# Optimization experiments

Hardware: AMD Instinct MI355X
Metric: run time of the kernel (lower is better)

## Reference

```python
import jax, jax.numpy as jnp
import numpy as np

EPS = 1e-5

def setup_inputs() -> dict:
    key = jax.random.key(0)
    k1, k2, k3, k4, k5 = jax.random.split(key, 5)
    x = jax.random.normal(k1, (2048, 64, 768), dtype=jnp.float32)
    ln_w = jnp.ones((768,), dtype=jnp.float32)
    ln_b = jnp.zeros((768,), dtype=jnp.float32)
    # nn.Linear default init: U(-1/sqrt(in), 1/sqrt(in))
    bound = 1.0 / np.sqrt(768.0)
    W = jax.random.uniform(k2, (64, 768), dtype=jnp.float32, minval=-bound, maxval=bound)
    b = jax.random.uniform(k3, (64,), dtype=jnp.float32, minval=-bound, maxval=bound)
    return {"x": x, "ln_w": ln_w, "ln_b": ln_b, "W": W, "b": b}

def reference(x, ln_w, ln_b, W, b):
    B = x.shape[0]
    # LayerNorm over last dim (768)
    mu = jnp.mean(x, axis=-1, keepdims=True)
    var = jnp.mean(jnp.square(x - mu), axis=-1, keepdims=True)
    xn = (x - mu) * jax.lax.rsqrt(var + EPS) * ln_w + ln_b
    # Linear 768 -> 64, then SiLU
    y = jnp.einsum('bch,oh->bco', xn, W) + b
    y = y * jax.nn.sigmoid(y)
    # unpatchify: [B,64,64] -> [B,8,8,4,4,4] -> permute(0,3,1,4,2,5) -> [B,4,32,32]
    y = y.reshape(B, 8, 8, 4, 4, 4)
    y = jnp.transpose(y, (0, 3, 1, 4, 2, 5))
    return y.reshape(B, 4, 32, 32)
```

## Files before the change

### kernel.cpp

```cpp
#include <hip/hip_runtime.h>
#include <hip/hip_bf16.h>
#include <cstdint>

typedef __attribute__((ext_vector_type(8))) short s16x8;
typedef __attribute__((ext_vector_type(4))) float f32x4;

union CV2 { __hip_bfloat162 h; uint32_t u; };

__global__ void prep_kernel(const float* __restrict__ W,
                            const float* __restrict__ lnw,
                            const float* __restrict__ lnb,
                            const float* __restrict__ bias,
                            __hip_bfloat16* __restrict__ Wb,
                            float* __restrict__ Ssum,
                            float* __restrict__ bp) {
    const int o = blockIdx.x;
    const int tid = threadIdx.x;
    float s = 0.f, bb = 0.f;
    for (int k = tid; k < 768; k += 256) {
        float wraw = W[o * 768 + k];
        float wv = lnw[k] * wraw;
        s += wv;
        bb += lnb[k] * wraw;
        int kk = k >> 5, rem = k & 31;
        int q = rem >> 3, j = rem & 7;
        int t = o >> 4, n = o & 15;
        int l = q * 16 + n;
        Wb[(kk * 4 + t) * 512 + l * 8 + j] = __float2bfloat16(wv);
    }
    __shared__ float rs[4], rb[4];
    for (int off = 32; off > 0; off >>= 1) {
        s  += __shfl_down(s, off);
        bb += __shfl_down(bb, off);
    }
    int wid = tid >> 6;
    if ((tid & 63) == 0) { rs[wid] = s; rb[wid] = bb; }
    __syncthreads();
    if (tid == 0) {
        Ssum[o] = rs[0] + rs[1] + rs[2] + rs[3];
        bp[o]   = bias[o] + rb[0] + rb[1] + rb[2] + rb[3];
    }
}

__global__ __launch_bounds__(256, 4) void fused_kernel(
        const float* __restrict__ x,
        const uint4* __restrict__ Wb4,
        const float* __restrict__ Ssum,
        const float* __restrict__ bp,
        float* __restrict__ out) {
    const int b   = blockIdx.x;
    const int tid = threadIdx.x;
    const int w   = tid >> 6;
    const int l   = tid & 63;
    const int q   = l >> 4;
    const int n   = l & 15;

    const float* xrow = x + (size_t)(b * 64 + w * 16 + n) * 768 + q * 8;

    f32x4 acc0 = {0.f, 0.f, 0.f, 0.f};
    f32x4 acc1 = acc0, acc2 = acc0, acc3 = acc0;
    float sum = 0.f, ssq = 0.f;

    #pragma unroll
    for (int kk = 0; kk < 24; kk++) {
        float4 v0 = *(const float4*)(xrow + kk * 32);
        float4 v1 = *(const float4*)(xrow + kk * 32 + 4);
        sum += ((v0.x + v0.y) + (v0.z + v0.w)) + ((v1.x + v1.y) + (v1.z + v1.w));
        ssq = fmaf(v0.x, v0.x, ssq); ssq = fmaf(v0.y, v0.y, ssq);
        ssq = fmaf(v0.z, v0.z, ssq); ssq = fmaf(v0.w, v0.w, ssq);
        ssq = fmaf(v1.x, v1.x, ssq); ssq = fmaf(v1.y, v1.y, ssq);
        ssq = fmaf(v1.z, v1.z, ssq); ssq = fmaf(v1.w, v1.w, ssq);

        CV2 c0, c1, c2, c3;
        c0.h = __float22bfloat162_rn(make_float2(v0.x, v0.y));
        c1.h = __float22bfloat162_rn(make_float2(v0.z, v0.w));
        c2.h = __float22bfloat162_rn(make_float2(v1.x, v1.y));
        c3.h = __float22bfloat162_rn(make_float2(v1.z, v1.w));
        s16x8 a = __builtin_bit_cast(s16x8, make_uint4(c0.u, c1.u, c2.u, c3.u));

        const uint4* wp = Wb4 + kk * 256 + l;
        s16x8 b0 = __builtin_bit_cast(s16x8, wp[0]);
        s16x8 b1 = __builtin_bit_cast(s16x8, wp[64]);
        s16x8 b2 = __builtin_bit_cast(s16x8, wp[128]);
        s16x8 b3 = __builtin_bit_cast(s16x8, wp[192]);

        acc0 = __builtin_amdgcn_mfma_f32_16x16x32_bf16(a, b0, acc0, 0, 0, 0);
        acc1 = __builtin_amdgcn_mfma_f32_16x16x32_bf16(a, b1, acc1, 0, 0, 0);
        acc2 = __builtin_amdgcn_mfma_f32_16x16x32_bf16(a, b2, acc2, 0, 0, 0);
        acc3 = __builtin_amdgcn_mfma_f32_16x16x32_bf16(a, b3, acc3, 0, 0, 0);
    }

    sum += __shfl_xor(sum, 16); sum += __shfl_xor(sum, 32);
    ssq += __shfl_xor(ssq, 16); ssq += __shfl_xor(ssq, 32);
    const float mu   = sum * (1.0f / 768.0f);
    const float var  = ssq * (1.0f / 768.0f) - mu * mu;
    const float rstd = rsqrtf(var + 1e-5f);

    float St[4], Bt[4];
    #pragma unroll
    for (int t = 0; t < 4; t++) {
        St[t] = Ssum[t * 16 + n];
        Bt[t] = bp[t * 16 + n];
    }

    __shared__ float sout[4096];
    const int o2 = (n >> 2) & 3;
    const int o3 = n & 3;
    #pragma unroll
    for (int r = 0; r < 4; r++) {
        float mu_r   = __shfl(mu,   q * 4 + r);
        float rstd_r = __shfl(rstd, q * 4 + r);
        int cc  = w * 16 + q * 4 + r;
        int c1i = cc >> 3, c2i = cc & 7;
        int base = (c1i * 4 + o2) * 32 + c2i * 4 + o3;
        float v[4] = {acc0[r], acc1[r], acc2[r], acc3[r]};
        #pragma unroll
        for (int t = 0; t < 4; t++) {
            float y = rstd_r * (v[t] - mu_r * St[t]) + Bt[t];
            y = y / (1.0f + __expf(-y));
            sout[t * 1024 + base] = y;
        }
    }
    __syncthreads();

    float* outp = out + (size_t)b * 4096;
    #pragma unroll
    for (int j = 0; j < 4; j++) {
        *(float4*)(outp + j * 1024 + tid * 4) =
            *(const float4*)(&sout[j * 1024 + tid * 4]);
    }
}

extern "C" void kernel_launch(void* const* d_in, const int* in_sizes, int n_in,
                              void* d_out, int out_size, void* d_ws, size_t ws_size,
                              hipStream_t stream) {
    const float* x    = (const float*)d_in[0];
    const float* lnw  = (const float*)d_in[1];
    const float* lnb  = (const float*)d_in[2];
    const float* W    = (const float*)d_in[3];
    const float* bias = (const float*)d_in[4];
    float* out = (float*)d_out;

    const int B = in_sizes[0] / (64 * 768);

    __hip_bfloat16* Wb = (__hip_bfloat16*)d_ws;
    float* Ssum = (float*)((char*)d_ws + 98304);
    float* bp   = (float*)((char*)d_ws + 98304 + 256);

    prep_kernel<<<64, 256, 0, stream>>>(W, lnw, lnb, bias, Wb, Ssum, bp);
    fused_kernel<<<B, 256, 0, stream>>>(x, (const uint4*)d_ws, Ssum, bp, out);
}
```

Before: 640.3 us.

## Process two batches per block and software-prefetch next k-step loads

Each block now handles two batch elements, with each wave covering 32 rows, so every W fragment load feeds eight MFMAs instead of four. The loop also preloads the next iteration's x and W fragments into registers while the current ones are used. The aim is more memory-level parallelism and hidden load latency in this bandwidth-bound LayerNorm+GEMM. The cost is higher register use, doubled shared memory per block, half as many blocks, and the assumption that B is even.

```diff
diff --git a/kernel.cpp b/kernel.cpp
--- a/kernel.cpp
+++ b/kernel.cpp
@@ -48,53 +48,93 @@
         const float* __restrict__ Ssum,
         const float* __restrict__ bp,
         float* __restrict__ out) {
-    const int b   = blockIdx.x;
+    const int bpair = blockIdx.x;
     const int tid = threadIdx.x;
     const int w   = tid >> 6;
     const int l   = tid & 63;
     const int q   = l >> 4;
     const int n   = l & 15;
 
-    const float* xrow = x + (size_t)(b * 64 + w * 16 + n) * 768 + q * 8;
-
-    f32x4 acc0 = {0.f, 0.f, 0.f, 0.f};
-    f32x4 acc1 = acc0, acc2 = acc0, acc3 = acc0;
-    float sum = 0.f, ssq = 0.f;
+    const float* xr0 = x + (size_t)(bpair * 128 + w * 32 + n) * 768 + q * 8;
+    const float* xr1 = xr0 + 16 * 768;
+
+    f32x4 acc00 = {0.f,0.f,0.f,0.f};
+    f32x4 acc01 = acc00, acc02 = acc00, acc03 = acc00;
+    f32x4 acc10 = acc00, acc11 = acc00, acc12 = acc00, acc13 = acc00;
+    float sum0 = 0.f, ssq0 = 0.f, sum1 = 0.f, ssq1 = 0.f;
+
+    const uint4* wbase = Wb4 + l;
+
+    float4 cx0a = *(const float4*)(xr0);
+    float4 cx0b = *(const float4*)(xr0 + 4);
+    float4 cx1a = *(const float4*)(xr1);
+    float4 cx1b = *(const float4*)(xr1 + 4);
+    uint4 cw0 = wbase[0], cw1 = wbase[64], cw2 = wbase[128], cw3 = wbase[192];
 
     #pragma unroll
     for (int kk = 0; kk < 24; kk++) {
-        float4 v0 = *(const float4*)(xrow + kk * 32);
-        float4 v1 = *(const float4*)(xrow + kk * 32 + 4);
-        sum += ((v0.x + v0.y) + (v0.z + v0.w)) + ((v1.x + v1.y) + (v1.z + v1.w));
-        ssq = fmaf(v0.x, v0.x, ssq); ssq = fmaf(v0.y, v0.y, ssq);
-        ssq = fmaf(v0.z, v0.z, ssq); ssq = fmaf(v0.w, v0.w, ssq);
-        ssq = fmaf(v1.x, v1.x, ssq); ssq = fmaf(v1.y, v1.y, ssq);
-        ssq = fmaf(v1.z, v1.z, ssq); ssq = fmaf(v1.w, v1.w, ssq);
+        float4 nx0a = cx0a, nx0b = cx0b, nx1a = cx1a, nx1b = cx1b;
+        uint4 nw0 = cw0, nw1 = cw1, nw2 = cw2, nw3 = cw3;
+        if (kk < 23) {
+            const float* p0 = xr0 + (kk + 1) * 32;
+            const float* p1 = xr1 + (kk + 1) * 32;
+            nx0a = *(const float4*)p0; nx0b = *(const float4*)(p0 + 4);
+            nx1a = *(const float4*)p1; nx1b = *(const float4*)(p1 + 4);
+            const uint4* wp = wbase + (kk + 1) * 256;
+            nw0 = wp[0]; nw1 = wp[64]; nw2 = wp[128]; nw3 = wp[192];
+        }
+
+        sum0 += ((cx0a.x + cx0a.y) + (cx0a.z + cx0a.w))
+              + ((cx0b.x + cx0b.y) + (cx0b.z + cx0b.w));
+        ssq0 = fmaf(cx0a.x, cx0a.x, ssq0); ssq0 = fmaf(cx0a.y, cx0a.y, ssq0);
+        ssq0 = fmaf(cx0a.z, cx0a.z, ssq0); ssq0 = fmaf(cx0a.w, cx0a.w, ssq0);
+        ssq0 = fmaf(cx0b.x, cx0b.x, ssq0); ssq0 = fmaf(cx0b.y, cx0b.y, ssq0);
+        ssq0 = fmaf(cx0b.z, cx0b.z, ssq0); ssq0 = fmaf(cx0b.w, cx0b.w, ssq0);
+        sum1 += ((cx1a.x + cx1a.y) + (cx1a.z + cx1a.w))
+              + ((cx1b.x + cx1b.y) + (cx1b.z + cx1b.w));
+        ssq1 = fmaf(cx1a.x, cx1a.x, ssq1); ssq1 = fmaf(cx1a.y, cx1a.y, ssq1);
+        ssq1 = fmaf(cx1a.z, cx1a.z, ssq1); ssq1 = fmaf(cx1a.w, cx1a.w, ssq1);
+        ssq1 = fmaf(cx1b.x, cx1b.x, ssq1); ssq1 = fmaf(cx1b.y, cx1b.y, ssq1);
+        ssq1 = fmaf(cx1b.z, cx1b.z, ssq1); ssq1 = fmaf(cx1b.w, cx1b.w, ssq1);
 
         CV2 c0, c1, c2, c3;
-        c0.h = __float22bfloat162_rn(make_float2(v0.x, v0.y));
-        c1.h = __float22bfloat162_rn(make_float2(v0.z, v0.w));
-        c2.h = __float22bfloat162_rn(make_float2(v1.x, v1.y));
-        c3.h = __float22bfloat162_rn(make_float2(v1.z, v1.w));
-        s16x8 a = __builtin_bit_cast(s16x8, make_uint4(c0.u, c1.u, c2.u, c3.u));
-
-        const uint4* wp = Wb4 + kk * 256 + l;
-        s16x8 b0 = __builtin_bit_cast(s16x8, wp[0]);
-        s16x8 b1 = __builtin_bit_cast(s16x8, wp[64]);
-        s16x8 b2 = __builtin_bit_cast(s16x8, wp[128]);
-        s16x8 b3 = __builtin_bit_cast(s16x8, wp[192]);
-
-        acc0 = __builtin_amdgcn_mfma_f32_16x16x32_bf16(a, b0, acc0, 0, 0, 0);
-        acc1 = __builtin_amdgcn_mfma_f32_16x16x32_bf16(a, b1, acc1, 0, 0, 0);
-        acc2 = __builtin_amdgcn_mfma_f32_16x16x32_bf16(a, b2, acc2, 0, 0, 0);
-        acc3 = __builtin_amdgcn_mfma_f32_16x16x32_bf16(a, b3, acc3, 0, 0, 0);
-    }
-
-    sum += __shfl_xor(sum, 16); sum += __shfl_xor(sum, 32);
-    ssq += __shfl_xor(ssq, 16); ssq += __shfl_xor(ssq, 32);
-    const float mu   = sum * (1.0f / 768.0f);
-    const float var  = ssq * (1.0f / 768.0f) - mu * mu;
-    const float rstd = rsqrtf(var + 1e-5f);
+        c0.h = __float22bfloat162_rn(make_float2(cx0a.x, cx0a.y));
+        c1.h = __float22bfloat162_rn(make_float2(cx0a.z, cx0a.w));
+        c2.h = __float22bfloat162_rn(make_float2(cx0b.x, cx0b.y));
+        c3.h = __float22bfloat162_rn(make_float2(cx0b.z, cx0b.w));
+        s16x8 a0 = __builtin_bit_cast(s16x8, make_uint4(c0.u, c1.u, c2.u, c3.u));
+        c0.h = __float22bfloat162_rn(make_float2(cx1a.x, cx1a.y));
+        c1.h = __float22bfloat162_rn(make_float2(cx1a.z, cx1a.w));
+        c2.h = __float22bfloat162_rn(make_float2(cx1b.x, cx1b.y));
+        c3.h = __float22bfloat162_rn(make_float2(cx1b.z, cx1b.w));
+        s16x8 a1 = __builtin_bit_cast(s16x8, make_uint4(c0.u, c1.u, c2.u, c3.u));
+
+        s16x8 b0 = __builtin_bit_cast(s16x8, cw0);
+        s16x8 b1 = __builtin_bit_cast(s16x8, cw1);
+        s16x8 b2 = __builtin_bit_cast(s16x8, cw2);
+        s16x8 b3 = __builtin_bit_cast(s16x8, cw3);
+
+        acc00 = __builtin_amdgcn_mfma_f32_16x16x32_bf16(a0, b0, acc00, 0, 0, 0);
+        acc01 = __builtin_amdgcn_mfma_f32_16x16x32_bf16(a0, b1, acc01, 0, 0, 0);
+        acc02 = __builtin_amdgcn_mfma_f32_16x16x32_bf16(a0, b2, acc02, 0, 0, 0);
+        acc03 = __builtin_amdgcn_mfma_f32_16x16x32_bf16(a0, b3, acc03, 0, 0, 0);
+        acc10 = __builtin_amdgcn_mfma_f32_16x16x32_bf16(a1, b0, acc10, 0, 0, 0);
+        acc11 = __builtin_amdgcn_mfma_f32_16x16x32_bf16(a1, b1, acc11, 0, 0, 0);
+        acc12 = __builtin_amdgcn_mfma_f32_16x16x32_bf16(a1, b2, acc12, 0, 0, 0);
+        acc13 = __builtin_amdgcn_mfma_f32_16x16x32_bf16(a1, b3, acc13, 0, 0, 0);
+
+        cx0a = nx0a; cx0b = nx0b; cx1a = nx1a; cx1b = nx1b;
+        cw0 = nw0; cw1 = nw1; cw2 = nw2; cw3 = nw3;
+    }
+
+    sum0 += __shfl_xor(sum0, 16); sum0 += __shfl_xor(sum0, 32);
+    ssq0 += __shfl_xor(ssq0, 16); ssq0 += __shfl_xor(ssq0, 32);
+    sum1 += __shfl_xor(sum1, 16); sum1 += __shfl_xor(sum1, 32);
+    ssq1 += __shfl_xor(ssq1, 16); ssq1 += __shfl_xor(ssq1, 32);
+    const float mu0   = sum0 * (1.0f / 768.0f);
+    const float rstd0 = rsqrtf(ssq0 * (1.0f / 768.0f) - mu0 * mu0 + 1e-5f);
+    const float mu1   = sum1 * (1.0f / 768.0f);
+    const float rstd1 = rsqrtf(ssq1 * (1.0f / 768.0f) - mu1 * mu1 + 1e-5f);
 
     float St[4], Bt[4];
     #pragma unroll
@@ -103,31 +143,44 @@
         Bt[t] = bp[t * 16 + n];
     }
 
-    __shared__ float sout[4096];
+    __shared__ float sout[2][4096];
+    const int bw = w >> 1;
+    const int h  = w & 1;
     const int o2 = (n >> 2) & 3;
     const int o3 = n & 3;
-    #pragma unroll
-    for (int r = 0; r < 4; r++) {
-        float mu_r   = __shfl(mu,   q * 4 + r);
-        float rstd_r = __shfl(rstd, q * 4 + r);
-        int cc  = w * 16 + q * 4 + r;
-        int c1i = cc >> 3, c2i = cc & 7;
-        int base = (c1i * 4 + o2) * 32 + c2i * 4 + o3;
-        float v[4] = {acc0[r], acc1[r], acc2[r], acc3[r]};
+
+    #pragma unroll
+    for (int g = 0; g < 2; g++) {
+        float mug   = g ? mu1   : mu0;
+        float rstdg = g ? rstd1 : rstd0;
+        f32x4 va[4];
+        if (g == 0) { va[0] = acc00; va[1] = acc01; va[2] = acc02; va[3] = acc03; }
+        else        { va[0] = acc10; va[1] = acc11; va[2] = acc12; va[3] = acc13; }
         #pragma unroll
-        for (int t = 0; t < 4; t++) {
-            float y = rstd_r * (v[t] - mu_r * St[t]) + Bt[t];
-            y = y / (1.0f + __expf(-y));
-            sout[t * 1024 + base] = y;
+        for (int r = 0; r < 4; r++) {
+            float mu_r   = __shfl(mug,   q * 4 + r);
+            float rstd_r = __shfl(rstdg, q * 4 + r);
+            int cc  = h * 32 + g * 16 + q * 4 + r;
+            int c1i = cc >> 3, c2i = cc & 7;
+            int base = (c1i * 4 + o2) * 32 + c2i * 4 + o3;
+            #pragma unroll
+            for (int t = 0; t < 4; t++) {
+                float y = rstd_r * (va[t][r] - mu_r * St[t]) + Bt[t];
+                y = y / (1.0f + __expf(-y));
+                sout[bw][t * 1024 + base] = y;
+            }
         }
     }
     __syncthreads();
 
-    float* outp = out + (size_t)b * 4096;
-    #pragma unroll
-    for (int j = 0; j < 4; j++) {
-        *(float4*)(outp + j * 1024 + tid * 4) =
-            *(const float4*)(&sout[j * 1024 + tid * 4]);
+    float* outp = out + (size_t)bpair * 8192;
+    #pragma unroll
+    for (int bb = 0; bb < 2; bb++) {
+        #pragma unroll
+        for (int j = 0; j < 4; j++) {
+            *(float4*)(outp + bb * 4096 + j * 1024 + tid * 4) =
+                *(const float4*)(&sout[bb][j * 1024 + tid * 4]);
+        }
     }
 }
 
@@ -148,5 +201,5 @@
     float* bp   = (float*)((char*)d_ws + 98304 + 256);
 
     prep_kernel<<<64, 256, 0, stream>>>(W, lnw, lnb, bias, Wb, Ssum, bp);
-    fused_kernel<<<B, 256, 0, stream>>>(x, (const uint4*)d_ws, Ssum, bp, out);
+    fused_kernel<<<B / 2, 256, 0, stream>>>(x, (const uint4*)d_ws, Ssum, bp, out);
 }
```

New measurement: 733.1 us. 14.5% more time.

## Stage x through double-buffered LDS with coalesced loads and software-pipelined chunks

Applied to the files above, without the earlier changes.

Before, each lane read strided 32-byte pieces of its own row straight from global memory. Now all 256 threads cooperatively load contiguous 128-column chunks of the 64x768 slab, convert them to bf16, and write them into a padded, double-buffered LDS tile. The next chunk's global loads are issued before the MFMAs on the current chunk, and the W fragments are prefetched one step ahead. LayerNorm statistics are now computed from the bf16-rounded values, which slightly changes numerics. LDS use of about 34 KB per block forces launch bounds to drop from 4 to 3 blocks, and each chunk adds a barrier.

```diff
diff --git a/kernel.cpp b/kernel.cpp
--- a/kernel.cpp
+++ b/kernel.cpp
@@ -42,7 +42,7 @@
     }
 }
 
-__global__ __launch_bounds__(256, 4) void fused_kernel(
+__global__ __launch_bounds__(256, 3) void fused_kernel(
         const float* __restrict__ x,
         const uint4* __restrict__ Wb4,
         const float* __restrict__ Ssum,
@@ -55,46 +55,91 @@
     const int q   = l >> 4;
     const int n   = l & 15;
 
-    const float* xrow = x + (size_t)(b * 64 + w * 16 + n) * 768 + q * 8;
+    __shared__ __align__(16) char lds[2 * 17408];
+
+    const float* xb = x + (size_t)b * 49152;
+    const int srow = tid >> 5;
+    const int u    = tid & 31;
+
+    float4 st[8];
+    #pragma unroll
+    for (int j = 0; j < 8; j++)
+        st[j] = *(const float4*)(xb + (j * 8 + srow) * 768 + u * 4);
+    #pragma unroll
+    for (int j = 0; j < 8; j++) {
+        CV2 lo, hi;
+        lo.h = __float22bfloat162_rn(make_float2(st[j].x, st[j].y));
+        hi.h = __float22bfloat162_rn(make_float2(st[j].z, st[j].w));
+        *(uint2*)(lds + (j * 8 + srow) * 272 + u * 8) = make_uint2(lo.u, hi.u);
+    }
+    __syncthreads();
 
     f32x4 acc0 = {0.f, 0.f, 0.f, 0.f};
     f32x4 acc1 = acc0, acc2 = acc0, acc3 = acc0;
     float sum = 0.f, ssq = 0.f;
+    const uint4* wbl = Wb4 + l;
 
     #pragma unroll
-    for (int kk = 0; kk < 24; kk++) {
-        float4 v0 = *(const float4*)(xrow + kk * 32);
-        float4 v1 = *(const float4*)(xrow + kk * 32 + 4);
-        sum += ((v0.x + v0.y) + (v0.z + v0.w)) + ((v1.x + v1.y) + (v1.z + v1.w));
-        ssq = fmaf(v0.x, v0.x, ssq); ssq = fmaf(v0.y, v0.y, ssq);
-        ssq = fmaf(v0.z, v0.z, ssq); ssq = fmaf(v0.w, v0.w, ssq);
-        ssq = fmaf(v1.x, v1.x, ssq); ssq = fmaf(v1.y, v1.y, ssq);
-        ssq = fmaf(v1.z, v1.z, ssq); ssq = fmaf(v1.w, v1.w, ssq);
+    for (int c = 0; c < 6; c++) {
+        if (c < 5) {
+            #pragma unroll
+            for (int j = 0; j < 8; j++)
+                st[j] = *(const float4*)(xb + (j * 8 + srow) * 768
+                                         + (c + 1) * 128 + u * 4);
+        }
 
-        CV2 c0, c1, c2, c3;
-        c0.h = __float22bfloat162_rn(make_float2(v0.x, v0.y));
-        c1.h = __float22bfloat162_rn(make_float2(v0.z, v0.w));
-        c2.h = __float22bfloat162_rn(make_float2(v1.x, v1.y));
-        c3.h = __float22bfloat162_rn(make_float2(v1.z, v1.w));
-        s16x8 a = __builtin_bit_cast(s16x8, make_uint4(c0.u, c1.u, c2.u, c3.u));
+        const char* bufp = lds + (c & 1) * 17408 + (w * 16 + n) * 272 + q * 16;
+        uint4 fr[4];
+        #pragma unroll
+        for (int s = 0; s < 4; s++) fr[s] = *(const uint4*)(bufp + s * 64);
 
-        const uint4* wp = Wb4 + kk * 256 + l;
-        s16x8 b0 = __builtin_bit_cast(s16x8, wp[0]);
-        s16x8 b1 = __builtin_bit_cast(s16x8, wp[64]);
-        s16x8 b2 = __builtin_bit_cast(s16x8, wp[128]);
-        s16x8 b3 = __builtin_bit_cast(s16x8, wp[192]);
+        const uint4* wpc = wbl + c * 1024;
+        uint4 wb0 = wpc[0], wb1 = wpc[64], wb2 = wpc[128], wb3 = wpc[192];
 
-        acc0 = __builtin_amdgcn_mfma_f32_16x16x32_bf16(a, b0, acc0, 0, 0, 0);
-        acc1 = __builtin_amdgcn_mfma_f32_16x16x32_bf16(a, b1, acc1, 0, 0, 0);
-        acc2 = __builtin_amdgcn_mfma_f32_16x16x32_bf16(a, b2, acc2, 0, 0, 0);
-        acc3 = __builtin_amdgcn_mfma_f32_16x16x32_bf16(a, b3, acc3, 0, 0, 0);
+        #pragma unroll
+        for (int s = 0; s < 4; s++) {
+            uint4 nb0, nb1, nb2, nb3;
+            if (s < 3) {
+                const uint4* wp = wpc + (s + 1) * 256;
+                nb0 = wp[0]; nb1 = wp[64]; nb2 = wp[128]; nb3 = wp[192];
+            }
+            union { uint4 u4; unsigned short us[8]; } fu; fu.u4 = fr[s];
+            #pragma unroll
+            for (int j = 0; j < 8; j++) {
+                float xv = __uint_as_float(((unsigned)fu.us[j]) << 16);
+                sum += xv;
+                ssq = fmaf(xv, xv, ssq);
+            }
+            s16x8 af = __builtin_bit_cast(s16x8, fr[s]);
+            acc0 = __builtin_amdgcn_mfma_f32_16x16x32_bf16(
+                       af, __builtin_bit_cast(s16x8, wb0), acc0, 0, 0, 0);
+            acc1 = __builtin_amdgcn_mfma_f32_16x16x32_bf16(
+                       af, __builtin_bit_cast(s16x8, wb1), acc1, 0, 0, 0);
+            acc2 = __builtin_amdgcn_mfma_f32_16x16x32_bf16(
+                       af, __builtin_bit_cast(s16x8, wb2), acc2, 0, 0, 0);
+            acc3 = __builtin_amdgcn_mfma_f32_16x16x32_bf16(
+                       af, __builtin_bit_cast(s16x8, wb3), acc3, 0, 0, 0);
+            if (s < 3) { wb0 = nb0; wb1 = nb1; wb2 = nb2; wb3 = nb3; }
+        }
+
+        if (c < 5) {
+            char* obuf = lds + ((c + 1) & 1) * 17408;
+            #pragma unroll
+            for (int j = 0; j < 8; j++) {
+                CV2 lo, hi;
+                lo.h = __float22bfloat162_rn(make_float2(st[j].x, st[j].y));
+                hi.h = __float22bfloat162_rn(make_float2(st[j].z, st[j].w));
+                *(uint2*)(obuf + (j * 8 + srow) * 272 + u * 8) =
+                    make_uint2(lo.u, hi.u);
+            }
+        }
+        __syncthreads();
     }
 
     sum += __shfl_xor(sum, 16); sum += __shfl_xor(sum, 32);
     ssq += __shfl_xor(ssq, 16); ssq += __shfl_xor(ssq, 32);
     const float mu   = sum * (1.0f / 768.0f);
-    const float var  = ssq * (1.0f / 768.0f) - mu * mu;
-    const float rstd = rsqrtf(var + 1e-5f);
+    const float rstd = rsqrtf(ssq * (1.0f / 768.0f) - mu * mu + 1e-5f);
 
     float St[4], Bt[4];
     #pragma unroll
@@ -103,9 +148,10 @@
         Bt[t] = bp[t * 16 + n];
     }
 
-    __shared__ float sout[4096];
+    float* sout = (float*)lds;
     const int o2 = (n >> 2) & 3;
     const int o3 = n & 3;
+    f32x4 va[4] = {acc0, acc1, acc2, acc3};
     #pragma unroll
     for (int r = 0; r < 4; r++) {
         float mu_r   = __shfl(mu,   q * 4 + r);
@@ -113,10 +159,9 @@
         int cc  = w * 16 + q * 4 + r;
         int c1i = cc >> 3, c2i = cc & 7;
         int base = (c1i * 4 + o2) * 32 + c2i * 4 + o3;
-        float v[4] = {acc0[r], acc1[r], acc2[r], acc3[r]};
         #pragma unroll
         for (int t = 0; t < 4; t++) {
-            float y = rstd_r * (v[t] - mu_r * St[t]) + Bt[t];
+            float y = rstd_r * (va[t][r] - mu_r * St[t]) + Bt[t];
             y = y / (1.0f + __expf(-y));
             sout[t * 1024 + base] = y;
         }
```

Result: faster. 559.7 us (-12.6%).
